# Performance work log

Measured on AMD Instinct MI355X. Metric: run time of the kernel, lower is better.

Reference implementation:

```python
import jax, jax.numpy as jnp
import numpy as np

DIM = 768
NUM_HEADS = 12
HEAD_DIM = DIM // NUM_HEADS


def setup_inputs() -> dict:
    key = jax.random.key(0)
    k1, k2, k3 = jax.random.split(key, 3)
    B, N, C = 1, 4096, DIM
    x = jax.random.normal(k1, (B, N, C), dtype=jnp.float32)
    w_qkv = jax.random.normal(k2, (C, 3 * C), dtype=jnp.float32) * (C ** -0.5)
    w_proj = jax.random.normal(k3, (C, C), dtype=jnp.float32) * (C ** -0.5)
    b_proj = jnp.zeros((C,), dtype=jnp.float32)
    return {"x": x, "w_qkv": w_qkv, "w_proj": w_proj, "b_proj": b_proj}


def reference(x, w_qkv, w_proj, b_proj):
    B, N, C = x.shape
    H, D = NUM_HEADS, HEAD_DIM
    scale = D ** -0.5
    # QKV projection (no bias), split into heads: [B, N, 3, H, D] -> bhnd
    qkv = (x @ w_qkv).reshape(B, N, 3, H, D)
    qkv = jnp.transpose(qkv, (2, 0, 3, 1, 4))  # [3, B, H, N, D]
    q, k, v = qkv[0], qkv[1], qkv[2]
    # world_size == 1 => all_gather is identity; full attention over N
    attn = jnp.einsum('bhnd,bhmd->bhnm', q * scale, k)
    attn = jax.nn.softmax(attn, axis=-1)
    out = jnp.einsum('bhnm,bhmd->bhnd', attn, v)
    out = jnp.transpose(out, (0, 2, 1, 3)).reshape(B, N, C)
    return out @ w_proj + b_proj
```

## Files before the change

kernel.cpp:

```cpp
#include <hip/hip_runtime.h>
#include <hip/hip_bf16.h>

#define NT 4096
#define CD 768
#define NH 12
#define HD 64
#define CQ 2304

typedef __bf16 bf;
typedef __bf16 v8bf __attribute__((ext_vector_type(8)));
typedef __bf16 v4bf __attribute__((ext_vector_type(4)));
typedef float  v4f  __attribute__((ext_vector_type(4)));

__device__ __forceinline__ void gld16(const bf* g, bf* l) {
  __builtin_amdgcn_global_load_lds(
      (__attribute__((address_space(1))) void*)g,
      (__attribute__((address_space(3))) void*)l,
      16, 0, 0);
}

__device__ __forceinline__ float fexp2(float x) {
#if defined(__HIP_DEVICE_COMPILE__)
  return __builtin_amdgcn_exp2f(x);
#else
  return x;
#endif
}

__global__ __launch_bounds__(256) void prep(
    const float* __restrict__ x, const float* __restrict__ wqkv,
    const float* __restrict__ wproj, bf* __restrict__ Xb,
    bf* __restrict__ WqkvT, bf* __restrict__ WpT) {
  __shared__ float tile[32][33];
  const int b = blockIdx.x, tid = threadIdx.x;
  if (b < 3072) {
    const int i = b * 256 + tid;
    const float4 v = ((const float4*)x)[i];
    bf o4[4] = {(bf)v.x, (bf)v.y, (bf)v.z, (bf)v.w};
    ((ushort4*)Xb)[i] = *(const ushort4*)o4;
    return;
  }
  const float* in;
  bf* out;
  int rows, cols, c0, r0;
  if (b < 4800) {
    const int t = b - 3072;
    in = wqkv; out = WqkvT; rows = CD; cols = CQ;
    c0 = (t % 72) * 32; r0 = (t / 72) * 32;
  } else {
    const int t = b - 4800;
    in = wproj; out = WpT; rows = CD; cols = CD;
    c0 = (t % 24) * 32; r0 = (t / 24) * 32;
  }
  const int tx = tid & 31, ty = tid >> 5;
#pragma unroll
  for (int j = 0; j < 32; j += 8)
    tile[ty + j][tx] = in[(size_t)(r0 + ty + j) * cols + (c0 + tx)];
  __syncthreads();
#pragma unroll
  for (int j = 0; j < 32; j += 8)
    out[(size_t)(c0 + ty + j) * rows + (r0 + tx)] = (bf)tile[tx][ty + j];
}

__global__ __launch_bounds__(256, 3) void gemm_qkv(
    const bf* __restrict__ A, const bf* __restrict__ Bt,
    bf* __restrict__ Qb, bf* __restrict__ Kb, bf* __restrict__ Vtb) {
  __shared__ __align__(16) bf As[2][128 * 32];
  __shared__ __align__(16) bf Bs[2][128 * 32];
  const int tid = threadIdx.x;
  const int lane = tid & 63, wave = tid >> 6;
  const int lane15 = lane & 15, quad = lane >> 4;
  const int waveM = wave & 1, waveN = wave >> 1;
  const int bm = blockIdx.x * 128;
  const int bn = blockIdx.y * 128;

  v4f acc[4][4];
#pragma unroll
  for (int i = 0; i < 4; ++i)
#pragma unroll
    for (int j = 0; j < 4; ++j) acc[i][j] = (v4f){0.f, 0.f, 0.f, 0.f};

  auto stageG = [&](int half, int k0) {
#pragma unroll
    for (int p = 0; p < 2; ++p) {
      const int t = tid + p * 256;
      const int r = t >> 2, c = (t & 3) * 8;
      gld16(A + (size_t)(bm + r) * CD + k0 + c, As[half] + t * 8);
    }
#pragma unroll
    for (int p = 0; p < 2; ++p) {
      const int t = tid + p * 256;
      const int r = t >> 2, c = (t & 3) * 8;
      gld16(Bt + (size_t)(bn + r) * CD + k0 + c, Bs[half] + t * 8);
    }
  };

  stageG(0, 0);
  asm volatile("s_waitcnt vmcnt(0)" ::: "memory");
  __syncthreads();

  for (int it = 0; it < CD / 32; ++it) {
    const int half = it & 1;
    if (it + 1 < CD / 32) stageG(half ^ 1, (it + 1) * 32);

    v8bf af[4], bfr[4];
#pragma unroll
    for (int mt = 0; mt < 4; ++mt)
      af[mt] = *(const v8bf*)(As[half] + (waveM * 64 + mt * 16 + lane15) * 32 + quad * 8);
#pragma unroll
    for (int nt = 0; nt < 4; ++nt)
      bfr[nt] = *(const v8bf*)(Bs[half] + (waveN * 64 + nt * 16 + lane15) * 32 + quad * 8);
#pragma unroll
    for (int mt = 0; mt < 4; ++mt)
#pragma unroll
      for (int nt = 0; nt < 4; ++nt)
        acc[mt][nt] = __builtin_amdgcn_mfma_f32_16x16x32_bf16(af[mt], bfr[nt], acc[mt][nt], 0, 0, 0);

    asm volatile("s_waitcnt vmcnt(0)" ::: "memory");
    __syncthreads();
  }

  const float QSCALE = 0.125f * 1.4426950408889634f;
#pragma unroll
  for (int mt = 0; mt < 4; ++mt) {
    const int rowB = bm + waveM * 64 + mt * 16 + quad * 4;
#pragma unroll
    for (int nt = 0; nt < 4; ++nt) {
      const int col = bn + waveN * 64 + nt * 16 + lane15;
      const int s = col / CD;
      const int rem = col - s * CD;
      const int h = rem >> 6, d = rem & 63;
      if (s == 2) {
        bf vp[4];
#pragma unroll
        for (int i = 0; i < 4; ++i) vp[i] = (bf)acc[mt][nt][i];
        const int pos = (rowB & ~31) + (((rowB & 15) >> 2) << 3) + (((rowB >> 4) & 1) << 2);
        *(uint2*)(Vtb + ((size_t)h * HD + d) * NT + pos) = *(const uint2*)vp;
      } else {
#pragma unroll
        for (int i = 0; i < 4; ++i) {
          const float v = acc[mt][nt][i];
          const int row = rowB + i;
          if (s == 0) Qb[((size_t)h * NT + row) * HD + d] = (bf)(v * QSCALE);
          else        Kb[((size_t)h * NT + row) * HD + d] = (bf)v;
        }
      }
    }
  }
}

__global__ __launch_bounds__(256, 3) void attn(
    const bf* __restrict__ Qb, const bf* __restrict__ Kb,
    const bf* __restrict__ Vtb, bf* __restrict__ Ob) {
  __shared__ __align__(16) char smem[49152];
  float* Red = (float*)smem;

  const int b = blockIdx.x;
  int h, qt;
  if (b < 512) { h = b & 7;        qt = b >> 3; }
  else { const int bb = b - 512; h = 8 + (bb & 3); qt = bb >> 2; }
  const int q0 = qt * 64;

  const int tid = threadIdx.x;
  const int wave = tid >> 6, lane = tid & 63;
  const int lane15 = lane & 15, quad = lane >> 4;

  const bf* Kh = Kb + (size_t)h * NT * HD;
  const bf* Vh = Vtb + (size_t)h * HD * NT;

  v8bf aQ[4][2];
#pragma unroll
  for (int sub = 0; sub < 4; ++sub) {
    const int qrow = q0 + sub * 16 + lane15;
    aQ[sub][0] = *(const v8bf*)(Qb + ((size_t)h * NT + qrow) * HD + quad * 8);
    aQ[sub][1] = *(const v8bf*)(Qb + ((size_t)h * NT + qrow) * HD + 32 + quad * 8);
  }

  v4f o[4][4];
#pragma unroll
  for (int sub = 0; sub < 4; ++sub)
#pragma unroll
    for (int dt = 0; dt < 4; ++dt) o[sub][dt] = (v4f){0.f, 0.f, 0.f, 0.f};
  float lsum[4] = {0.f, 0.f, 0.f, 0.f};

  auto stageK = [&](int half, int kt) {
    bf* Kdst = (bf*)(smem + half * 16384);
#pragma unroll
    for (int p = 0; p < 4; ++p) {
      const int L = p * 256 + tid;
      const int r = L >> 3, u = L & 7;
      gld16(Kh + (size_t)(kt + r) * HD + ((u ^ (r & 7)) << 3), Kdst + L * 8);
    }
  };
  auto stageV = [&](int kt) {
    bf* Vdst = (bf*)(smem + 32768);
#pragma unroll
    for (int p = 0; p < 4; ++p) {
      const int L = p * 256 + tid;
      const int d = L >> 4, u = L & 15;
      gld16(Vh + (size_t)d * NT + kt + ((u ^ (d & 15)) << 3), Vdst + L * 8);
    }
  };

  stageK(0, 0);
  stageV(0);
  stageK(1, 128);
  asm volatile("s_waitcnt vmcnt(4)" ::: "memory");
  __syncthreads();

  const int NIT = NT / 128;
  for (int it = 0; it < NIT; ++it) {
    const int half = it & 1;
    if (it > 0) {
      if (it < NIT - 1) asm volatile("s_waitcnt vmcnt(8)" ::: "memory");
      else              asm volatile("s_waitcnt vmcnt(4)" ::: "memory");
    }
    const bf* Kbuf = (const bf*)(smem + half * 16384);
    const bf* Vbuf = (const bf*)(smem + 32768);

    v4bf aPlo[4], aPhi[4];
#pragma unroll
    for (int e = 0; e < 2; ++e) {
      const int k = (wave * 2 + e) * 16 + lane15;
      const int k7 = k & 7;
      const v8bf bk0 = *(const v8bf*)(Kbuf + k * 64 + ((quad ^ k7) << 3));
      const v8bf bk1 = *(const v8bf*)(Kbuf + k * 64 + (((quad ^ 4) ^ k7) << 3));
#pragma unroll
      for (int sub = 0; sub < 4; ++sub) {
        v4f z = (v4f){0.f, 0.f, 0.f, 0.f};
        z = __builtin_amdgcn_mfma_f32_16x16x32_bf16(bk0, aQ[sub][0], z, 0, 0, 0);
        z = __builtin_amdgcn_mfma_f32_16x16x32_bf16(bk1, aQ[sub][1], z, 0, 0, 0);
        v4bf p4;
#pragma unroll
        for (int r = 0; r < 4; ++r) {
          const float p = fexp2(z[r]);
          lsum[sub] += p;
          p4[r] = (bf)p;
        }
        if (e == 0) aPlo[sub] = p4; else aPhi[sub] = p4;
      }
    }

    if (it < NIT - 1) asm volatile("s_waitcnt vmcnt(4)" ::: "memory");
    else              asm volatile("s_waitcnt vmcnt(0)" ::: "memory");

#pragma unroll
    for (int dt = 0; dt < 4; ++dt) {
      const int d = dt * 16 + lane15;
      const v8bf bv = *(const v8bf*)(Vbuf + d * 128 + (((wave * 4 + quad) ^ lane15) << 3));
#pragma unroll
      for (int sub = 0; sub < 4; ++sub) {
        const v8bf aP8 = __builtin_shufflevector(aPlo[sub], aPhi[sub], 0, 1, 2, 3, 4, 5, 6, 7);
        o[sub][dt] = __builtin_amdgcn_mfma_f32_16x16x32_bf16(aP8, bv, o[sub][dt], 0, 0, 0);
      }
    }

    __syncthreads();
    if (it + 1 < NIT) stageV((it + 1) * 128);
    if (it + 2 < NIT) stageK(half, (it + 2) * 128);
  }

#pragma unroll
  for (int sub = 0; sub < 4; ++sub) {
    lsum[sub] += __shfl_xor(lsum[sub], 16, 64);
    lsum[sub] += __shfl_xor(lsum[sub], 32, 64);
  }

#pragma unroll
  for (int sp = 0; sp < 2; ++sp) {
    __syncthreads();
#pragma unroll
    for (int sl = 0; sl < 2; ++sl) {
      const int s = sp * 2 + sl;
      float* reg = Red + (wave * 2 + sl) * 1024;
#pragma unroll
      for (int dt = 0; dt < 4; ++dt)
        *(v4f*)(reg + dt * 256 + lane15 * 16 + quad * 4) = o[s][dt];
      if (quad == 0) Red[8192 + (wave * 2 + sl) * 16 + lane15] = lsum[s];
    }
    __syncthreads();
    const int wlo = sp * 2;
    if (wave == wlo || wave == wlo + 1) {
      const int sl = wave - wlo;
      const int s = sp * 2 + sl;
      float den = 0.f;
#pragma unroll
      for (int wv = 0; wv < 4; ++wv) den += Red[8192 + (wv * 2 + sl) * 16 + lane15];
      const float linv = 1.f / den;
#pragma unroll
      for (int dt = 0; dt < 4; ++dt) {
        v4f sum = (v4f){0.f, 0.f, 0.f, 0.f};
#pragma unroll
        for (int wv = 0; wv < 4; ++wv)
          sum += *(const v4f*)(Red + (wv * 2 + sl) * 1024 + dt * 256 + lane15 * 16 + quad * 4);
#pragma unroll
        for (int i = 0; i < 4; ++i) {
          const float linv_i = __shfl(linv, quad * 4 + i, 64);
          const int row = q0 + s * 16 + quad * 4 + i;
          Ob[(size_t)row * CD + h * HD + dt * 16 + lane15] = (bf)(sum[i] * linv_i);
        }
      }
    }
  }
}

__global__ __launch_bounds__(256, 4) void gemm_proj(
    const bf* __restrict__ A, const bf* __restrict__ Bt,
    const float* __restrict__ bias, float* __restrict__ out) {
  __shared__ __align__(16) bf As[2][64 * 32];
  __shared__ __align__(16) bf Bs[2][128 * 32];
  const int tid = threadIdx.x;
  const int lane = tid & 63, wave = tid >> 6;
  const int lane15 = lane & 15, quad = lane >> 4;
  const int bm = blockIdx.x * 64;
  const int bn = blockIdx.y * 128;

  v4f acc[4][2];
#pragma unroll
  for (int i = 0; i < 4; ++i)
#pragma unroll
    for (int j = 0; j < 2; ++j) acc[i][j] = (v4f){0.f, 0.f, 0.f, 0.f};

  auto stageG = [&](int half, int k0) {
    {
      const int r = tid >> 2, c = (tid & 3) * 8;
      gld16(A + (size_t)(bm + r) * CD + k0 + c, As[half] + tid * 8);
    }
#pragma unroll
    for (int p = 0; p < 2; ++p) {
      const int t = tid + p * 256;
      const int r = t >> 2, c = (t & 3) * 8;
      gld16(Bt + (size_t)(bn + r) * CD + k0 + c, Bs[half] + t * 8);
    }
  };

  stageG(0, 0);
  asm volatile("s_waitcnt vmcnt(0)" ::: "memory");
  __syncthreads();

  for (int it = 0; it < CD / 32; ++it) {
    const int half = it & 1;
    if (it + 1 < CD / 32) stageG(half ^ 1, (it + 1) * 32);

    v8bf af[4], bfr[2];
#pragma unroll
    for (int mt = 0; mt < 4; ++mt)
      af[mt] = *(const v8bf*)(As[half] + (mt * 16 + lane15) * 32 + quad * 8);
#pragma unroll
    for (int nt = 0; nt < 2; ++nt)
      bfr[nt] = *(const v8bf*)(Bs[half] + (wave * 32 + nt * 16 + lane15) * 32 + quad * 8);
#pragma unroll
    for (int mt = 0; mt < 4; ++mt)
#pragma unroll
      for (int nt = 0; nt < 2; ++nt)
        acc[mt][nt] = __builtin_amdgcn_mfma_f32_16x16x32_bf16(af[mt], bfr[nt], acc[mt][nt], 0, 0, 0);

    asm volatile("s_waitcnt vmcnt(0)" ::: "memory");
    __syncthreads();
  }

#pragma unroll
  for (int mt = 0; mt < 4; ++mt) {
    const int rowB = bm + mt * 16 + quad * 4;
#pragma unroll
    for (int nt = 0; nt < 2; ++nt) {
      const int col = bn + wave * 32 + nt * 16 + lane15;
      const float bcol = bias[col];
#pragma unroll
      for (int i = 0; i < 4; ++i)
        out[(size_t)(rowB + i) * CD + col] = acc[mt][nt][i] + bcol;
    }
  }
}

extern "C" void kernel_launch(void* const* d_in, const int* in_sizes, int n_in,
                              void* d_out, int out_size, void* d_ws, size_t ws_size,
                              hipStream_t stream) {
  const float* x     = (const float*)d_in[0];
  const float* wqkv  = (const float*)d_in[1];
  const float* wproj = (const float*)d_in[2];
  const float* bproj = (const float*)d_in[3];
  float* out = (float*)d_out;

  bf* ws    = (bf*)d_ws;
  bf* Xb    = ws;  ws += (size_t)NT * CD;
  bf* WqkvT = ws;  ws += (size_t)CQ * CD;
  bf* WpT   = ws;  ws += (size_t)CD * CD;
  bf* Qb    = ws;  ws += (size_t)NH * NT * HD;
  bf* Kb    = ws;  ws += (size_t)NH * NT * HD;
  bf* Vtb   = ws;  ws += (size_t)NH * NT * HD;
  bf* Ob    = ws;  ws += (size_t)NT * CD;

  prep<<<5376, 256, 0, stream>>>(x, wqkv, wproj, Xb, WqkvT, WpT);
  gemm_qkv<<<dim3(NT / 128, CQ / 128), 256, 0, stream>>>(Xb, WqkvT, Qb, Kb, Vtb);
  attn<<<768, 256, 0, stream>>>(Qb, Kb, Vtb, Ob);
  gemm_proj<<<dim3(NT / 64, CD / 128), 256, 0, stream>>>(Ob, WpT, bproj, out);
}
```

Baseline: 196.0 us.

## Restructure QKV GEMM and attention LDS staging into simpler swizzled buffers

The QKV GEMM switches from a double-buffered K-step of 32 to a single-buffered K-step of 64, using XOR-swizzled LDS rows. Each iteration now loads, waits and then computes, with no overlap between loads and MFMA. The attention kernel replaces its staggered pipeline (K two tiles ahead, single V buffer, fine-grained vmcnt waits) with a plain double buffer of K+V per tile. That needs 64KB of LDS per block and drops launch bounds from 3 to 2 blocks per SM. This simplifies synchronisation but reduces occupancy and load/compute overlap.

```diff
diff --git a/kernel.cpp b/kernel.cpp
--- a/kernel.cpp
+++ b/kernel.cpp
@@ -65,8 +65,8 @@
 __global__ __launch_bounds__(256, 3) void gemm_qkv(
     const bf* __restrict__ A, const bf* __restrict__ Bt,
     bf* __restrict__ Qb, bf* __restrict__ Kb, bf* __restrict__ Vtb) {
-  __shared__ __align__(16) bf As[2][128 * 32];
-  __shared__ __align__(16) bf Bs[2][128 * 32];
+  __shared__ __align__(16) bf As[128 * 64];
+  __shared__ __align__(16) bf Bs[128 * 64];
   const int tid = threadIdx.x;
   const int lane = tid & 63, wave = tid >> 6;
   const int lane15 = lane & 15, quad = lane >> 4;
@@ -80,43 +80,44 @@
 #pragma unroll
     for (int j = 0; j < 4; ++j) acc[i][j] = (v4f){0.f, 0.f, 0.f, 0.f};
 
-  auto stageG = [&](int half, int k0) {
-#pragma unroll
-    for (int p = 0; p < 2; ++p) {
+  for (int k0 = 0; k0 < CD; k0 += 64) {
+#pragma unroll
+    for (int p = 0; p < 4; ++p) {
       const int t = tid + p * 256;
-      const int r = t >> 2, c = (t & 3) * 8;
-      gld16(A + (size_t)(bm + r) * CD + k0 + c, As[half] + t * 8);
-    }
-#pragma unroll
-    for (int p = 0; p < 2; ++p) {
+      const int r = t >> 3, u = t & 7;
+      gld16(A + (size_t)(bm + r) * CD + k0 + ((u ^ (r & 7)) << 3), As + t * 8);
+    }
+#pragma unroll
+    for (int p = 0; p < 4; ++p) {
       const int t = tid + p * 256;
-      const int r = t >> 2, c = (t & 3) * 8;
-      gld16(Bt + (size_t)(bn + r) * CD + k0 + c, Bs[half] + t * 8);
-    }
-  };
-
-  stageG(0, 0);
-  asm volatile("s_waitcnt vmcnt(0)" ::: "memory");
-  __syncthreads();
-
-  for (int it = 0; it < CD / 32; ++it) {
-    const int half = it & 1;
-    if (it + 1 < CD / 32) stageG(half ^ 1, (it + 1) * 32);
-
-    v8bf af[4], bfr[4];
+      const int r = t >> 3, u = t & 7;
+      gld16(Bt + (size_t)(bn + r) * CD + k0 + ((u ^ (r & 7)) << 3), Bs + t * 8);
+    }
+    asm volatile("s_waitcnt vmcnt(0)" ::: "memory");
+    __syncthreads();
+
+    v8bf af[4][2], bfr[4][2];
+#pragma unroll
+    for (int mt = 0; mt < 4; ++mt) {
+      const int rr = waveM * 64 + mt * 16 + lane15;
+      const int r7 = rr & 7;
+      af[mt][0] = *(const v8bf*)(As + rr * 64 + ((quad ^ r7) << 3));
+      af[mt][1] = *(const v8bf*)(As + rr * 64 + (((quad ^ 4) ^ r7) << 3));
+    }
+#pragma unroll
+    for (int nt = 0; nt < 4; ++nt) {
+      const int rr = waveN * 64 + nt * 16 + lane15;
+      const int r7 = rr & 7;
+      bfr[nt][0] = *(const v8bf*)(Bs + rr * 64 + ((quad ^ r7) << 3));
+      bfr[nt][1] = *(const v8bf*)(Bs + rr * 64 + (((quad ^ 4) ^ r7) << 3));
+    }
 #pragma unroll
     for (int mt = 0; mt < 4; ++mt)
-      af[mt] = *(const v8bf*)(As[half] + (waveM * 64 + mt * 16 + lane15) * 32 + quad * 8);
-#pragma unroll
-    for (int nt = 0; nt < 4; ++nt)
-      bfr[nt] = *(const v8bf*)(Bs[half] + (waveN * 64 + nt * 16 + lane15) * 32 + quad * 8);
-#pragma unroll
-    for (int mt = 0; mt < 4; ++mt)
-#pragma unroll
-      for (int nt = 0; nt < 4; ++nt)
-        acc[mt][nt] = __builtin_amdgcn_mfma_f32_16x16x32_bf16(af[mt], bfr[nt], acc[mt][nt], 0, 0, 0);
-
-    asm volatile("s_waitcnt vmcnt(0)" ::: "memory");
+#pragma unroll
+      for (int nt = 0; nt < 4; ++nt) {
+        acc[mt][nt] = __builtin_amdgcn_mfma_f32_16x16x32_bf16(af[mt][0], bfr[nt][0], acc[mt][nt], 0, 0, 0);
+        acc[mt][nt] = __builtin_amdgcn_mfma_f32_16x16x32_bf16(af[mt][1], bfr[nt][1], acc[mt][nt], 0, 0, 0);
+      }
     __syncthreads();
   }
 
@@ -149,10 +150,10 @@
   }
 }
 
-__global__ __launch_bounds__(256, 3) void attn(
+__global__ __launch_bounds__(256, 2) void attn(
     const bf* __restrict__ Qb, const bf* __restrict__ Kb,
     const bf* __restrict__ Vtb, bf* __restrict__ Ob) {
-  __shared__ __align__(16) char smem[49152];
+  __shared__ __align__(16) char smem[65536];
   float* Red = (float*)smem;
 
   const int b = blockIdx.x;
@@ -183,17 +184,15 @@
     for (int dt = 0; dt < 4; ++dt) o[sub][dt] = (v4f){0.f, 0.f, 0.f, 0.f};
   float lsum[4] = {0.f, 0.f, 0.f, 0.f};
 
-  auto stageK = [&](int half, int kt) {
-    bf* Kdst = (bf*)(smem + half * 16384);
+  auto stage = [&](int half, int kt) {
+    bf* Kdst = (bf*)(smem + half * 32768);
+    bf* Vdst = (bf*)(smem + half * 32768 + 16384);
 #pragma unroll
     for (int p = 0; p < 4; ++p) {
       const int L = p * 256 + tid;
       const int r = L >> 3, u = L & 7;
       gld16(Kh + (size_t)(kt + r) * HD + ((u ^ (r & 7)) << 3), Kdst + L * 8);
     }
-  };
-  auto stageV = [&](int kt) {
-    bf* Vdst = (bf*)(smem + 32768);
 #pragma unroll
     for (int p = 0; p < 4; ++p) {
       const int L = p * 256 + tid;
@@ -202,21 +201,16 @@
     }
   };
 
-  stageK(0, 0);
-  stageV(0);
-  stageK(1, 128);
-  asm volatile("s_waitcnt vmcnt(4)" ::: "memory");
+  stage(0, 0);
+  asm volatile("s_waitcnt vmcnt(0)" ::: "memory");
   __syncthreads();
 
-  const int NIT = NT / 128;
-  for (int it = 0; it < NIT; ++it) {
+  for (int it = 0; it < NT / 128; ++it) {
     const int half = it & 1;
-    if (it > 0) {
-      if (it < NIT - 1) asm volatile("s_waitcnt vmcnt(8)" ::: "memory");
-      else              asm volatile("s_waitcnt vmcnt(4)" ::: "memory");
-    }
-    const bf* Kbuf = (const bf*)(smem + half * 16384);
-    const bf* Vbuf = (const bf*)(smem + 32768);
+    if (it + 1 < NT / 128) stage(half ^ 1, (it + 1) * 128);
+
+    const bf* Kbuf = (const bf*)(smem + half * 32768);
+    const bf* Vbuf = (const bf*)(smem + half * 32768 + 16384);
 
     v4bf aPlo[4], aPhi[4];
 #pragma unroll
@@ -241,9 +235,6 @@
       }
     }
 
-    if (it < NIT - 1) asm volatile("s_waitcnt vmcnt(4)" ::: "memory");
-    else              asm volatile("s_waitcnt vmcnt(0)" ::: "memory");
-
 #pragma unroll
     for (int dt = 0; dt < 4; ++dt) {
       const int d = dt * 16 + lane15;
@@ -255,9 +246,8 @@
       }
     }
 
-    __syncthreads();
-    if (it + 1 < NIT) stageV((it + 1) * 128);
-    if (it + 2 < NIT) stageK(half, (it + 2) * 128);
+    asm volatile("s_waitcnt vmcnt(0)" ::: "memory");
+    __syncthreads();
   }
 
 #pragma unroll
```

Result: faster. 172.2 us (-12.2%).
